# Performance work log

Measured on AMD Instinct MI355X. Metric: run time of the kernel, lower is better.

Reference implementation:

```python
import jax, jax.numpy as jnp
import numpy as np

COUNT = 8
OUT_F = 32
IN_F = 1024
QN, QP = -128, 127  # int8 LSQ range used by nnue-pytorch


def _grad_scale(x, s):
    # forward: x ; backward: grad * s
    return x * s + jax.lax.stop_gradient(x - x * s)


def _round_pass(x):
    # forward: round(x) ; backward: identity (STE)
    return x + jax.lax.stop_gradient(jnp.round(x) - x)


def quantized_weight(weight, log_alpha_w):
    # LSQ (learned step size quantization), per-output-row step size
    alpha = jnp.exp(log_alpha_w)[:, None]                    # [O*C, 1]
    g = 1.0 / np.sqrt(float(weight.size) * QP)
    alpha = _grad_scale(alpha, jnp.asarray(g, weight.dtype))
    w_s = jnp.clip(weight / alpha, QN, QP)
    return _round_pass(w_s) * alpha                          # [O*C, I]


def setup_inputs() -> dict:
    key = jax.random.key(0)
    k1, k2, k3, k4, k5 = jax.random.split(key, 5)
    B = 8192
    x = jax.random.normal(k1, (B, IN_F), dtype=jnp.float32)
    ls_indices = jax.random.randint(k2, (B,), 0, COUNT).astype(jnp.int64)
    weight = jax.random.normal(k3, (COUNT * OUT_F, IN_F), dtype=jnp.float32) * 0.02
    bias = jax.random.normal(k4, (COUNT * OUT_F,), dtype=jnp.float32) * 0.01
    log_alpha_w = jax.random.normal(k5, (COUNT * OUT_F,), dtype=jnp.float32) * 0.1 - 5.0
    return {"x": x, "ls_indices": ls_indices, "weight": weight,
            "bias": bias, "log_alpha_w": log_alpha_w}


def reference(x, ls_indices, weight, bias, log_alpha_w):
    wq = quantized_weight(weight, log_alpha_w)               # [C*O, I]
    w_r = wq.reshape(COUNT, OUT_F, IN_F)                     # [C, O, I]
    b_r = bias.reshape(COUNT, OUT_F)                         # [C, O]
    idx = ls_indices.astype(jnp.int32)
    w_sel = w_r[idx]                                         # [B, O, I] gather
    b_sel = b_r[idx]                                         # [B, O]
    out = jnp.einsum("boi,bi->bo", w_sel, x)                # per-sample matvec
    return out + b_sel
```

## Files before the change

kernel.cpp:

```cpp
#include <hip/hip_runtime.h>


#define IN_F   1024
#define OUT_F  32
#define NCLS   8
#define NB     8192
#define KSPLIT 8
#define KCH    (IN_F / KSPLIT)
#define GRIDX  40

typedef __attribute__((ext_vector_type(8))) __bf16 bf16x8;
typedef __attribute__((ext_vector_type(4))) float  f32x4;

__device__ __forceinline__ unsigned short f2bf(float f) {
    unsigned int u = __builtin_bit_cast(unsigned int, f);
    u += 0x7FFFu + ((u >> 16) & 1u);
    return (unsigned short)(u >> 16);
}

__device__ __forceinline__ bf16x8 pack8(float4 v0, float4 v1) {
    union { unsigned short u[8]; bf16x8 v; } r;
    r.u[0] = f2bf(v0.x); r.u[1] = f2bf(v0.y); r.u[2] = f2bf(v0.z); r.u[3] = f2bf(v0.w);
    r.u[4] = f2bf(v1.x); r.u[5] = f2bf(v1.y); r.u[6] = f2bf(v1.z); r.u[7] = f2bf(v1.w);
    return r.v;
}

__global__ __launch_bounds__(1024) void prep_kernel(
    const float* __restrict__ weight, const float* __restrict__ law,
    const unsigned int* __restrict__ lsw, const float* __restrict__ bias,
    float* __restrict__ alf, unsigned short* __restrict__ wq,
    int* __restrict__ counts, unsigned short* __restrict__ buckets,
    float* __restrict__ out)
{
    int t = threadIdx.x;
    if (blockIdx.x < 64) {
        int row = blockIdx.x * 4 + (t >> 8);
        int c4  = t & 255;
        float a = expf(law[row]);
        if (c4 == 0) alf[row] = a;
        float4 v = ((const float4*)(weight + (size_t)row * IN_F))[c4];
        ushort4 p;
        p.x = f2bf(rintf(fminf(fmaxf(v.x / a, -128.f), 127.f)));
        p.y = f2bf(rintf(fminf(fmaxf(v.y / a, -128.f), 127.f)));
        p.z = f2bf(rintf(fminf(fmaxf(v.z / a, -128.f), 127.f)));
        p.w = f2bf(rintf(fminf(fmaxf(v.w / a, -128.f), 127.f)));
        ((ushort4*)(wq + (size_t)row * IN_F))[c4] = p;
        return;
    }
    if (blockIdx.x < 96) {
        int base = (int)(blockIdx.x - 64) * 256;
        __shared__ int s_is64b;
        if (t == 0) s_is64b = 1;
        __syncthreads();
        if (t < 256 && lsw[2 * (base + t) + 1] != 0u) atomicAnd(&s_is64b, 0);
        __syncthreads();
        int is64 = s_is64b;
        #pragma unroll
        for (int p = 0; p < 2; ++p) {
            int row  = base + p * 128 + (t >> 3);
            int quad = t & 7;
            int c = is64 ? (int)lsw[2 * row] : (int)lsw[row];
            ((float4*)(out + (size_t)row * OUT_F))[quad] =
                ((const float4*)(bias + c * OUT_F))[quad];
        }
        return;
    }
    int c = (int)blockIdx.x - 96;
    int lane = t & 63, wv = t >> 6;
    __shared__ int s_is64;
    __shared__ int wtot[16];
    __shared__ int wbase[16];
    if (t == 0) s_is64 = 1;
    __syncthreads();
    int bad = 0;
    #pragma unroll
    for (int j = 0; j < 4; ++j) bad |= (lsw[2 * (j * 1024 + t) + 1] != 0u);
    if (bad) atomicAnd(&s_is64, 0);
    __syncthreads();
    int is64 = s_is64;
    unsigned int match = 0;
    int cnt = 0;
    #pragma unroll
    for (int j = 0; j < 8; ++j) {
        int b = j * 1024 + t;
        int cl = is64 ? (int)lsw[2 * b] : (int)lsw[b];
        if (cl == c) { match |= 1u << j; ++cnt; }
    }
    int inc = cnt;
    #pragma unroll
    for (int d = 1; d < 64; d <<= 1) {
        int o = __shfl_up(inc, d);
        if (lane >= d) inc += o;
    }
    if (lane == 63) wtot[wv] = inc;
    __syncthreads();
    if (t < 16) {
        int b0 = 0;
        for (int w2 = 0; w2 < t; ++w2) b0 += wtot[w2];
        wbase[t] = b0;
        if (t == 15) counts[c] = b0 + wtot[15];
    }
    __syncthreads();
    int pos = wbase[wv] + inc - cnt;
    unsigned short* bk = buckets + c * NB;
    #pragma unroll
    for (int j = 0; j < 8; ++j) {
        if ((match >> j) & 1u) bk[pos++] = (unsigned short)(j * 1024 + t);
    }
}

__global__ __launch_bounds__(128) void gemm_kernel(
    const float* __restrict__ x, const float* __restrict__ alf,
    const unsigned short* __restrict__ wq,
    const int* __restrict__ counts, const unsigned short* __restrict__ buckets,
    float* __restrict__ out)
{
    int c  = blockIdx.y;
    int kq = blockIdx.z;
    int cnt = counts[c];
    int ntiles = (cnt + 15) >> 4;
    if ((int)blockIdx.x * 2 >= ntiles) return;
    int t = threadIdx.x;
    int wave = t >> 6, lane = t & 63;
    int fr = lane & 15, fq = lane >> 4;
    int k0 = kq * KCH;

    const unsigned short* wrow0 = wq + (size_t)(c * OUT_F + fr) * IN_F + k0 + fq * 8;
    const unsigned short* wrow1 = wrow0 + 16 * IN_F;
    bf16x8 Bf0[KCH / 32], Bf1[KCH / 32];
    #pragma unroll
    for (int kk = 0; kk < KCH / 32; ++kk) {
        Bf0[kk] = *(const bf16x8*)(wrow0 + kk * 32);
        Bf1[kk] = *(const bf16x8*)(wrow1 + kk * 32);
    }
    float a0 = alf[c * OUT_F + fr];
    float a1 = alf[c * OUT_F + 16 + fr];

    for (int tile = blockIdx.x * 2 + wave; tile < ntiles; tile += GRIDX * 2) {
        int start = tile * 16;
        int nvalid = min(16, cnt - start);
        int j = min(fr, nvalid - 1);
        int srow = (int)buckets[c * NB + start + j];
        const float* xr = x + (size_t)srow * IN_F + k0 + fq * 8;
        f32x4 acc0 = {0.f, 0.f, 0.f, 0.f};
        f32x4 acc1 = {0.f, 0.f, 0.f, 0.f};
        #pragma unroll
        for (int kk = 0; kk < KCH / 32; ++kk) {
            float4 v0 = *(const float4*)(xr + kk * 32);
            float4 v1 = *(const float4*)(xr + kk * 32 + 4);
            bf16x8 a = pack8(v0, v1);
            acc0 = __builtin_amdgcn_mfma_f32_16x16x32_bf16(a, Bf0[kk], acc0, 0, 0, 0);
            acc1 = __builtin_amdgcn_mfma_f32_16x16x32_bf16(a, Bf1[kk], acc1, 0, 0, 0);
        }
        #pragma unroll
        for (int reg = 0; reg < 4; ++reg) {
            int m = fq * 4 + reg;
            int sr = __shfl(srow, m);
            if (m < nvalid) {
                atomicAdd(&out[(size_t)sr * OUT_F + fr],      acc0[reg] * a0);
                atomicAdd(&out[(size_t)sr * OUT_F + 16 + fr], acc1[reg] * a1);
            }
        }
    }
}

extern "C" void kernel_launch(void* const* d_in, const int* in_sizes, int n_in,
                              void* d_out, int out_size, void* d_ws, size_t ws_size,
                              hipStream_t stream)
{
    (void)in_sizes; (void)n_in; (void)out_size; (void)ws_size;
    const float*        x      = (const float*)d_in[0];
    const unsigned int* ls     = (const unsigned int*)d_in[1];
    const float*        weight = (const float*)d_in[2];
    const float*        bias   = (const float*)d_in[3];
    const float*        law    = (const float*)d_in[4];
    float*              out    = (float*)d_out;

    char* ws = (char*)d_ws;
    int*            counts  = (int*)ws;
    float*          alf     = (float*)(ws + 64);
    unsigned short* wq      = (unsigned short*)(ws + 64 + 1024);
    unsigned short* buckets = (unsigned short*)(ws + 64 + 1024 + 524288);

    prep_kernel<<<104, 1024, 0, stream>>>(
        weight, law, ls, bias, alf, wq, counts, buckets, out);
    gemm_kernel<<<dim3(GRIDX, NCLS, KSPLIT), 128, 0, stream>>>(
        x, alf, wq, counts, buckets, out);
}
```

Before: 90.62 us.

## Reduce K-split partials in shared memory instead of global atomics, fuse bias

The K-split moves from the grid's z dimension into the 8 waves of a 512-thread block. Each wave's MFMA partial sums are written to shared memory and reduced there, and a single plain store writes the scaled result plus bias. This removes the global atomicAdds and the separate bias-initialization pass in the prep kernel. In exchange each tile now needs block-wide barriers, and the grid size changes to 68 blocks per class.

After: 91.06 us. Within noise of the previous version (+0.5%).

```diff
diff --git a/kernel.cpp b/kernel.cpp
--- a/kernel.cpp
+++ b/kernel.cpp
@@ -7,7 +7,7 @@
 #define NB     8192
 #define KSPLIT 8
 #define KCH    (IN_F / KSPLIT)
-#define GRIDX  40
+#define GRIDX  68
 
 typedef __attribute__((ext_vector_type(8))) __bf16 bf16x8;
 typedef __attribute__((ext_vector_type(4))) float  f32x4;
@@ -27,10 +27,9 @@
 
 __global__ __launch_bounds__(1024) void prep_kernel(
     const float* __restrict__ weight, const float* __restrict__ law,
-    const unsigned int* __restrict__ lsw, const float* __restrict__ bias,
+    const unsigned int* __restrict__ lsw,
     float* __restrict__ alf, unsigned short* __restrict__ wq,
-    int* __restrict__ counts, unsigned short* __restrict__ buckets,
-    float* __restrict__ out)
+    int* __restrict__ counts, unsigned short* __restrict__ buckets)
 {
     int t = threadIdx.x;
     if (blockIdx.x < 64) {
@@ -47,25 +46,7 @@
         ((ushort4*)(wq + (size_t)row * IN_F))[c4] = p;
         return;
     }
-    if (blockIdx.x < 96) {
-        int base = (int)(blockIdx.x - 64) * 256;
-        __shared__ int s_is64b;
-        if (t == 0) s_is64b = 1;
-        __syncthreads();
-        if (t < 256 && lsw[2 * (base + t) + 1] != 0u) atomicAnd(&s_is64b, 0);
-        __syncthreads();
-        int is64 = s_is64b;
-        #pragma unroll
-        for (int p = 0; p < 2; ++p) {
-            int row  = base + p * 128 + (t >> 3);
-            int quad = t & 7;
-            int c = is64 ? (int)lsw[2 * row] : (int)lsw[row];
-            ((float4*)(out + (size_t)row * OUT_F))[quad] =
-                ((const float4*)(bias + c * OUT_F))[quad];
-        }
-        return;
-    }
-    int c = (int)blockIdx.x - 96;
+    int c = (int)blockIdx.x - 64;
     int lane = t & 63, wv = t >> 6;
     __shared__ int s_is64;
     __shared__ int wtot[16];
@@ -109,21 +90,24 @@
     }
 }
 
-__global__ __launch_bounds__(128) void gemm_kernel(
+__global__ __launch_bounds__(512) void gemm_kernel(
     const float* __restrict__ x, const float* __restrict__ alf,
-    const unsigned short* __restrict__ wq,
+    const unsigned short* __restrict__ wq, const float* __restrict__ bias,
     const int* __restrict__ counts, const unsigned short* __restrict__ buckets,
     float* __restrict__ out)
 {
-    int c  = blockIdx.y;
-    int kq = blockIdx.z;
+    int c = blockIdx.y;
     int cnt = counts[c];
     int ntiles = (cnt + 15) >> 4;
-    if ((int)blockIdx.x * 2 >= ntiles) return;
+    if ((int)blockIdx.x >= ntiles) return;
+
+    __shared__ float lred[KSPLIT][16][33];
+    __shared__ int   sid[16];
+
     int t = threadIdx.x;
-    int wave = t >> 6, lane = t & 63;
+    int wv = t >> 6, lane = t & 63;
     int fr = lane & 15, fq = lane >> 4;
-    int k0 = kq * KCH;
+    int k0 = wv * KCH;
 
     const unsigned short* wrow0 = wq + (size_t)(c * OUT_F + fr) * IN_F + k0 + fq * 8;
     const unsigned short* wrow1 = wrow0 + 16 * IN_F;
@@ -133,14 +117,18 @@
         Bf0[kk] = *(const bf16x8*)(wrow0 + kk * 32);
         Bf1[kk] = *(const bf16x8*)(wrow1 + kk * 32);
     }
-    float a0 = alf[c * OUT_F + fr];
-    float a1 = alf[c * OUT_F + 16 + fr];
+    int em = t >> 5, eo = t & 31;
+    float av = alf[c * OUT_F + eo];
+    float bv = bias[c * OUT_F + eo];
 
-    for (int tile = blockIdx.x * 2 + wave; tile < ntiles; tile += GRIDX * 2) {
+    for (int tile = blockIdx.x; tile < ntiles; tile += GRIDX) {
         int start = tile * 16;
         int nvalid = min(16, cnt - start);
-        int j = min(fr, nvalid - 1);
-        int srow = (int)buckets[c * NB + start + j];
+        if (t < 16)
+            sid[t] = (int)buckets[c * NB + start + min(t, nvalid - 1)];
+        __syncthreads();
+
+        int srow = sid[fr];
         const float* xr = x + (size_t)srow * IN_F + k0 + fq * 8;
         f32x4 acc0 = {0.f, 0.f, 0.f, 0.f};
         f32x4 acc1 = {0.f, 0.f, 0.f, 0.f};
@@ -155,12 +143,17 @@
         #pragma unroll
         for (int reg = 0; reg < 4; ++reg) {
             int m = fq * 4 + reg;
-            int sr = __shfl(srow, m);
-            if (m < nvalid) {
-                atomicAdd(&out[(size_t)sr * OUT_F + fr],      acc0[reg] * a0);
-                atomicAdd(&out[(size_t)sr * OUT_F + 16 + fr], acc1[reg] * a1);
-            }
+            lred[wv][m][fr]      = acc0[reg];
+            lred[wv][m][16 + fr] = acc1[reg];
         }
+        __syncthreads();
+        if (em < nvalid) {
+            float s = 0.f;
+            #pragma unroll
+            for (int w2 = 0; w2 < KSPLIT; ++w2) s += lred[w2][em][eo];
+            out[(size_t)sid[em] * OUT_F + eo] = s * av + bv;
+        }
+        __syncthreads();
     }
 }
 
@@ -182,8 +175,8 @@
     unsigned short* wq      = (unsigned short*)(ws + 64 + 1024);
     unsigned short* buckets = (unsigned short*)(ws + 64 + 1024 + 524288);
 
-    prep_kernel<<<104, 1024, 0, stream>>>(
-        weight, law, ls, bias, alf, wq, counts, buckets, out);
-    gemm_kernel<<<dim3(GRIDX, NCLS, KSPLIT), 128, 0, stream>>>(
-        x, alf, wq, counts, buckets, out);
+    prep_kernel<<<72, 1024, 0, stream>>>(
+        weight, law, ls, alf, wq, counts, buckets);
+    gemm_kernel<<<dim3(GRIDX, NCLS), 512, 0, stream>>>(
+        x, alf, wq, bias, counts, buckets, out);
 }
```
